# Performance work log

Hardware: AMD Instinct MI355X
Metric: run time of the kernel (lower is better)

The kernel has to match this reference:

```python
import jax, jax.numpy as jnp
import numpy as np

N_NODES, N_EDGES, D_IN, D_OUT = 50000, 800000, 64, 64
N_REL, N_TIME = 500, 1000


def setup_inputs() -> dict:
    key = jax.random.key(0)
    ks = jax.random.split(key, 14)
    xavier = lambda k, shape: jax.random.normal(k, shape, jnp.float32) * np.sqrt(2.0 / (shape[0] + shape[1])) * np.sqrt(2.0)
    return {
        "x": jax.random.normal(ks[0], (N_NODES, D_IN), jnp.float32),
        "rel_repr": jax.random.normal(ks[1], (N_REL, D_IN), jnp.float32),
        "time_emds": jax.random.normal(ks[2], (N_TIME, D_IN), jnp.float32),
        "src": jax.random.randint(ks[3], (N_EDGES,), 0, N_NODES),
        "dst": jax.random.randint(ks[4], (N_EDGES,), 0, N_NODES),
        "etype": jax.random.randint(ks[5], (N_EDGES,), 0, N_REL),
        "etime": jax.random.randint(ks[6], (N_EDGES,), 0, N_TIME),
        "trans_w": xavier(ks[7], (D_IN, D_OUT)),
        "loop_w": xavier(ks[8], (D_IN, D_OUT)),
        "w_rel": xavier(ks[9], (D_IN, D_OUT)),
        "attn_h": xavier(ks[10], (D_IN, 1)),
        "attn_t": xavier(ks[11], (D_IN, 1)),
        "attn_r": xavier(ks[12], (D_IN, 1)),
        "attn_ts": xavier(ks[13], (D_IN, 1)),
    }


def reference(x, rel_repr, time_emds, src, dst, etype, etime,
              trans_w, loop_w, w_rel, attn_h, attn_t, attn_r, attn_ts):
    n = x.shape[0]
    # per-node / per-rel / per-time scalar attention projections
    h_att = (x @ attn_h)[:, 0]          # [N]
    t_att = (x @ attn_t)[:, 0]          # [N]
    r_att = (rel_repr @ attn_r)[:, 0]   # [R]
    ts_att = (time_emds @ attn_ts)[:, 0]  # [T]
    # edge attention logits + edge_softmax grouped by destination node
    e = jax.nn.leaky_relu(h_att[src] - t_att[dst] + r_att[etype] + ts_att[etime], 0.1)  # [E]
    m = jax.ops.segment_max(e, dst, num_segments=n)
    ex = jnp.exp(e - m[dst])
    den = jax.ops.segment_sum(ex, dst, num_segments=n)
    att = (ex / den[dst])[:, None]      # [E,1]
    # message: (head + time) * (rel + time) -> trans_w -> weighted scatter-sum to dst
    time_emd = time_emds[etime]         # [E,D]
    edge_data = (x[src] + time_emd) * (rel_repr[etype] + time_emd)
    msg = (edge_data @ trans_w) * att   # [E,D_out]
    h = jax.ops.segment_sum(msg, dst, num_segments=n)
    x_out = h + x @ loop_w
    rel_out = rel_repr @ w_rel
    return (x_out, rel_out)
```

## Files before the change

kernel.cpp:

```cpp
#include <hip/hip_runtime.h>
#include <hip/hip_bf16.h>

#define N_NODES 50000
#define N_EDGES 800000
#define D 64
#define N_REL 500
#define N_TIME 1000
#define SLOTS 64
#define NODE_BLOCKS ((N_NODES + 63) / 64)
#define REL_BLOCKS  ((N_REL + 63) / 64)

#define CB 64
#define NCB ((N_NODES + CB - 1) / CB)
#define FR 64
#define NFB ((N_NODES + FR - 1) / FR)
#define SCAP 2048
#define BINCAP 8
#define BTILE 4096
#define LSLOT 48

__device__ __forceinline__ float bf2f(unsigned short u) {
    union { unsigned int i; float f; } v;
    v.i = ((unsigned int)u) << 16;
    return v.f;
}

__global__ void proj_kernel(const float* __restrict__ x,
                            const float* __restrict__ rel,
                            const float* __restrict__ tim,
                            const float* __restrict__ ah,
                            const float* __restrict__ at,
                            const float* __restrict__ ar,
                            const float* __restrict__ ats,
                            float* __restrict__ h_att, float* __restrict__ t_att,
                            float* __restrict__ r_att, float* __restrict__ ts_att,
                            unsigned short* __restrict__ x_bf,
                            int* __restrict__ cursor) {
    int gid = blockIdx.x * blockDim.x + threadIdx.x;
    if (gid < NCB) cursor[gid] = 0;
    int wave = gid >> 6;
    int lane = threadIdx.x & 63;
    const int total = N_NODES + N_REL + N_TIME;
    if (wave >= total) return;
    if (wave < N_NODES) {
        float xv = x[wave * D + lane];
        __hip_bfloat16 b = __float2bfloat16(xv);
        x_bf[wave * D + lane] = *(unsigned short*)&b;
        float s1 = xv * ah[lane];
        float s2 = xv * at[lane];
        for (int off = 32; off; off >>= 1) {
            s1 += __shfl_down(s1, off);
            s2 += __shfl_down(s2, off);
        }
        if (lane == 0) { h_att[wave] = s1; t_att[wave] = s2; }
    } else if (wave < N_NODES + N_REL) {
        int r = wave - N_NODES;
        float v = rel[r * D + lane] * ar[lane];
        for (int off = 32; off; off >>= 1) v += __shfl_down(v, off);
        if (lane == 0) r_att[r] = v;
    } else {
        int t = wave - N_NODES - N_REL;
        float v = tim[t * D + lane] * ats[lane];
        for (int off = 32; off; off >>= 1) v += __shfl_down(v, off);
        if (lane == 0) ts_att[t] = v;
    }
}

__global__ __launch_bounds__(512)
void bin_kernel(const int* __restrict__ src, const int* __restrict__ dst,
                const int* __restrict__ etype, const int* __restrict__ etime,
                const float* __restrict__ h_att, const float* __restrict__ t_att,
                const float* __restrict__ r_att, const float* __restrict__ ts_att,
                int* __restrict__ cursor, int4* __restrict__ stage) {
    __shared__ int4 bins[NCB][BINCAP];
    __shared__ int bcnt[NCB];
    int t = threadIdx.x;
    for (int k = t; k < NCB; k += 512) bcnt[k] = 0;
    __syncthreads();

    int e0 = blockIdx.x * BTILE;
    for (int j = 0; j < 8; j++) {
        int e = e0 + j * 512 + t;
        if (e < N_EDGES) {
            int s = src[e], d = dst[e], r = etype[e], tt = etime[e];
            float lg = h_att[s] - t_att[d] + r_att[r] + ts_att[tt];
            float lr = lg > 0.f ? lg : 0.1f * lg;
            float ex = __expf(lr);
            unsigned exb = __float_as_uint(ex);
            int4 rec;
            rec.x = (int)((exb & ~7u) | (unsigned)(s & 7));
            rec.y = (int)(((unsigned)(s >> 3) << 19) | ((unsigned)r << 10) | (unsigned)tt);
            rec.z = d;
            rec.w = 0;
            int k = d >> 6;
            int pos = atomicAdd(&bcnt[k], 1);
            if (pos < BINCAP) {
                bins[k][pos] = rec;
            } else {
                int g = atomicAdd(&cursor[k], 1);
                if (g < SCAP) stage[(size_t)k * SCAP + g] = rec;
            }
        }
    }
    __syncthreads();
    for (int k = t; k < NCB; k += 512) {
        int c = bcnt[k];
        if (c > BINCAP) c = BINCAP;
        if (c > 0) {
            int base = atomicAdd(&cursor[k], c);
            for (int i = 0; i < c; i++) {
                int g = base + i;
                if (g < SCAP) stage[(size_t)k * SCAP + g] = bins[k][i];
            }
        }
    }
}

__global__ __launch_bounds__(512)
void node_fused_kernel(const unsigned short* __restrict__ x_bf,
                       const float* __restrict__ rel,
                       const float* __restrict__ tim,
                       const float* __restrict__ x,
                       const float* __restrict__ trans_w,
                       const float* __restrict__ loop_w,
                       const int* __restrict__ cursor,
                       const int4* __restrict__ stage,
                       float* __restrict__ out) {
    __shared__ int2  lslot_s[FR * LSLOT];
    __shared__ int   lcnt[FR];
    __shared__ float Wt[D * D];
    __shared__ float Wl[D * D];
    __shared__ float Xt[FR * D];
    float* At = (float*)lslot_s;

    int tid = threadIdx.x;
    int base = blockIdx.x * FR;
    int pb = blockIdx.x;

    for (int i = tid; i < FR; i += 512) lcnt[i] = 0;
    {
        int2 z = make_int2(0, 0);
        for (int i = tid; i < FR * LSLOT; i += 512) lslot_s[i] = z;
    }
    for (int j = 0; j < 2; j++) {
        int idx = (tid + 512 * j) * 4;
        *(float4*)(Wt + idx) = *(const float4*)(trans_w + idx);
        *(float4*)(Wl + idx) = *(const float4*)(loop_w + idx);
    }
    for (int j = 0; j < 2; j++) {
        int lin = tid + 512 * j;
        int rr = lin >> 4;
        int k4 = (lin & 15) << 2;
        int gr = base + rr; if (gr >= N_NODES) gr = N_NODES - 1;
        *(float4*)(Xt + rr * D + k4) = *(const float4*)(x + (size_t)gr * D + k4);
    }
    __syncthreads();

    int n = cursor[pb];
    if (n > SCAP) n = SCAP;
    for (int i = tid; i < n; i += 512) {
        int4 rec = stage[(size_t)pb * SCAP + i];
        int ln = rec.z - base;
        if ((unsigned)ln < FR) {
            int pos = atomicAdd(&lcnt[ln], 1);
            if (pos < LSLOT) lslot_s[ln * LSLOT + pos] = make_int2(rec.x, rec.y);
        }
    }
    __syncthreads();

    int lane = tid & 63;
    int wv = tid >> 6;
    int qw = lane >> 4;
    int ql = lane & 15;
    float4 acc4[8];

#pragma unroll
    for (int j = 0; j < 8; j++) {
        int ln = wv + j * 8;
        int deg = lcnt[ln];
        if (deg > LSLOT) deg = LSLOT;

        float ex = 0.f;
        if (lane < deg) {
            int2 pl = lslot_s[ln * LSLOT + lane];
            ex = __uint_as_float((unsigned)pl.x & ~7u);
        }
        float den = ex;
        for (int off = 32; off; off >>= 1) den += __shfl_xor(den, off);
        float rden = 1.f / den;

        const int2* row = lslot_s + ln * LSLOT;
        float4 acc = make_float4(0.f, 0.f, 0.f, 0.f);
        for (int i = 0; i < deg; i += 8) {
            int eA = i + qw;
            int eB = i + 4 + qw;
            int2 pA = row[eA];
            int2 pB = row[eB];
            unsigned pxA = (unsigned)pA.x, pyA = (unsigned)pA.y;
            unsigned pxB = (unsigned)pB.x, pyB = (unsigned)pB.y;
            float attA = (eA < deg) ? __uint_as_float(pxA & ~7u) * rden : 0.f;
            float attB = (eB < deg) ? __uint_as_float(pxB & ~7u) * rden : 0.f;
            int sA = (int)(((pyA >> 19) << 3) | (pxA & 7u));
            int rA = (int)((pyA >> 10) & 511u);
            int tA = (int)(pyA & 1023u);
            int sB = (int)(((pyB >> 19) << 3) | (pxB & 7u));
            int rB = (int)((pyB >> 10) & 511u);
            int tB = (int)(pyB & 1023u);
            float4  teA = *(const float4*)(tim + tA * D + ql * 4);
            ushort4 xbA = *(const ushort4*)(x_bf + sA * D + ql * 4);
            float4  rlA = *(const float4*)(rel + rA * D + ql * 4);
            float4  teB = *(const float4*)(tim + tB * D + ql * 4);
            ushort4 xbB = *(const ushort4*)(x_bf + sB * D + ql * 4);
            float4  rlB = *(const float4*)(rel + rB * D + ql * 4);
            acc.x += attA * (bf2f(xbA.x) + teA.x) * (rlA.x + teA.x);
            acc.y += attA * (bf2f(xbA.y) + teA.y) * (rlA.y + teA.y);
            acc.z += attA * (bf2f(xbA.z) + teA.z) * (rlA.z + teA.z);
            acc.w += attA * (bf2f(xbA.w) + teA.w) * (rlA.w + teA.w);
            acc.x += attB * (bf2f(xbB.x) + teB.x) * (rlB.x + teB.x);
            acc.y += attB * (bf2f(xbB.y) + teB.y) * (rlB.y + teB.y);
            acc.z += attB * (bf2f(xbB.z) + teB.z) * (rlB.z + teB.z);
            acc.w += attB * (bf2f(xbB.w) + teB.w) * (rlB.w + teB.w);
        }
        for (int off = 16; off <= 32; off <<= 1) {
            acc.x += __shfl_xor(acc.x, off);
            acc.y += __shfl_xor(acc.y, off);
            acc.z += __shfl_xor(acc.z, off);
            acc.w += __shfl_xor(acc.w, off);
        }
        acc4[j] = acc;
    }
    __syncthreads();

#pragma unroll
    for (int j = 0; j < 8; j++) {
        if (qw == 0) {
            int ln = wv + j * 8;
            *(float4*)(At + ln * D + ql * 4) = acc4[j];
        }
    }
    __syncthreads();

    int c4 = ql << 2;
    int r0 = wv * 8 + qw * 2;
    float acc[2][4];
    for (int i = 0; i < 2; i++)
        for (int c = 0; c < 4; c++) acc[i][c] = 0.f;

    for (int k = 0; k < D; k += 4) {
        float wt[4][4], wl[4][4];
        for (int kk = 0; kk < 4; kk++) {
            *(float4*)&wt[kk][0] = *(const float4*)(Wt + (k + kk) * D + c4);
            *(float4*)&wl[kk][0] = *(const float4*)(Wl + (k + kk) * D + c4);
        }
        for (int i = 0; i < 2; i++) {
            float a[4], xv[4];
            *(float4*)&a[0]  = *(const float4*)(At + (r0 + i) * D + k);
            *(float4*)&xv[0] = *(const float4*)(Xt + (r0 + i) * D + k);
            for (int c = 0; c < 4; c++) {
                float s = acc[i][c];
                for (int kk = 0; kk < 4; kk++)
                    s += a[kk] * wt[kk][c] + xv[kk] * wl[kk][c];
                acc[i][c] = s;
            }
        }
    }
    for (int i = 0; i < 2; i++) {
        int gr = base + r0 + i;
        if (gr < N_NODES)
            *(float4*)(out + (size_t)gr * D + c4) = *(float4*)&acc[i][0];
    }
}

__global__ __launch_bounds__(256)
void rel_gemm_kernel(const float* __restrict__ rel,
                     const float* __restrict__ w_rel,
                     float* __restrict__ out) {
    __shared__ float Wa[D * D];
    __shared__ float At[64 * D];
    int t = threadIdx.x;
    int row0 = blockIdx.x * 64;

    for (int j = 0; j < 4; j++) {
        int idx = (t + 256 * j) * 4;
        *(float4*)(Wa + idx) = *(const float4*)(w_rel + idx);
    }
    for (int j = 0; j < 4; j++) {
        int lin = t + 256 * j;
        int rr = lin >> 4;
        int k4 = (lin & 15) << 2;
        int gr = row0 + rr; if (gr >= N_REL) gr = N_REL - 1;
        *(float4*)(At + rr * D + k4) = *(const float4*)(rel + (size_t)gr * D + k4);
    }
    __syncthreads();

    int lane = t & 63;
    int wv = t >> 6;
    int c4 = (lane & 15) << 2;
    int r0 = wv * 16 + (lane >> 4) * 4;

    float acc[4][4];
    for (int i = 0; i < 4; i++)
        for (int c = 0; c < 4; c++) acc[i][c] = 0.f;

    for (int k = 0; k < D; k += 4) {
        float wt[4][4];
        for (int kk = 0; kk < 4; kk++)
            *(float4*)&wt[kk][0] = *(const float4*)(Wa + (k + kk) * D + c4);
        for (int i = 0; i < 4; i++) {
            float a[4];
            *(float4*)&a[0] = *(const float4*)(At + (r0 + i) * D + k);
            for (int c = 0; c < 4; c++) {
                float s = acc[i][c];
                for (int kk = 0; kk < 4; kk++)
                    s += a[kk] * wt[kk][c];
                acc[i][c] = s;
            }
        }
    }
    for (int i = 0; i < 4; i++) {
        int gr = row0 + r0 + i;
        if (gr < N_REL)
            *(float4*)(out + (size_t)(N_NODES + gr) * D + c4) = *(float4*)&acc[i][0];
    }
}

__global__ void build_kernel(const int* __restrict__ src, const int* __restrict__ dst,
                             const int* __restrict__ etype, const int* __restrict__ etime,
                             const float* __restrict__ h_att, const float* __restrict__ t_att,
                             const float* __restrict__ r_att, const float* __restrict__ ts_att,
                             int* __restrict__ cnt, int2* __restrict__ payload) {
    int e = blockIdx.x * blockDim.x + threadIdx.x;
    if (e >= N_EDGES) return;
    int s = src[e], d = dst[e], r = etype[e], t = etime[e];
    float lg = h_att[s] - t_att[d] + r_att[r] + ts_att[t];
    float lr = lg > 0.f ? lg : 0.1f * lg;
    float ex = __expf(lr);
    unsigned exb = __float_as_uint(ex);
    int2 pl;
    pl.x = (int)((exb & ~7u) | (unsigned)(s & 7));
    pl.y = (int)(((unsigned)(s >> 3) << 19) | ((unsigned)r << 10) | (unsigned)t);
    int pos = atomicAdd(&cnt[d], 1);
    if (pos < SLOTS) payload[(d << 6) + pos] = pl;
}

__global__ void node_gather_kernel(const unsigned short* __restrict__ x_bf,
                                   const float* __restrict__ rel,
                                   const float* __restrict__ tim,
                                   const int* __restrict__ cnt,
                                   const int2* __restrict__ payload,
                                   float* __restrict__ agg) {
    int d = (blockIdx.x * blockDim.x + threadIdx.x) >> 6;
    int lane = threadIdx.x & 63;
    if (d >= N_NODES) return;
    int deg = cnt[d];
    if (deg > SLOTS) deg = SLOTS;
    int s_l = 0, r_l = 0, t_l = 0;
    float ex = 0.f;
    if (lane < deg) {
        int2 pl = payload[(d << 6) + lane];
        unsigned px = (unsigned)pl.x;
        unsigned py = (unsigned)pl.y;
        ex = __uint_as_float(px & ~7u);
        s_l = (int)(((py >> 19) << 3) | (px & 7u));
        r_l = (int)((py >> 10) & 511u);
        t_l = (int)(py & 1023u);
    }
    float den = ex;
    for (int off = 32; off; off >>= 1) den += __shfl_xor(den, off);
    float att_l = (lane < deg) ? ex / den : 0.f;
    int qw = lane >> 4;
    int ql = lane & 15;
    float4 acc = make_float4(0.f, 0.f, 0.f, 0.f);
    for (int i = 0; i < deg; i += 4) {
        int ei = i + qw;
        int s = __shfl(s_l, ei);
        int r = __shfl(r_l, ei);
        int t = __shfl(t_l, ei);
        float att = __shfl(att_l, ei);
        float4  te = *(const float4*)(tim + t * D + ql * 4);
        ushort4 xb = *(const ushort4*)(x_bf + s * D + ql * 4);
        float4  rl = *(const float4*)(rel + r * D + ql * 4);
        acc.x += att * (bf2f(xb.x) + te.x) * (rl.x + te.x);
        acc.y += att * (bf2f(xb.y) + te.y) * (rl.y + te.y);
        acc.z += att * (bf2f(xb.z) + te.z) * (rl.z + te.z);
        acc.w += att * (bf2f(xb.w) + te.w) * (rl.w + te.w);
    }
    for (int off = 16; off <= 32; off <<= 1) {
        acc.x += __shfl_xor(acc.x, off);
        acc.y += __shfl_xor(acc.y, off);
        acc.z += __shfl_xor(acc.z, off);
        acc.w += __shfl_xor(acc.w, off);
    }
    if (qw == 0)
        *(float4*)(agg + (d << 7) + ql * 4) = acc;
}

__global__ __launch_bounds__(256, 2)
void out_gemm_kernel(const float* __restrict__ agg,
                     const float* __restrict__ x,
                     const float* __restrict__ rel,
                     const float* __restrict__ trans_w,
                     const float* __restrict__ loop_w,
                     const float* __restrict__ w_rel,
                     float* __restrict__ out, int astride) {
    __shared__ float Wa[D * D];
    __shared__ float Wb[D * D];
    __shared__ float At[64 * D];
    __shared__ float Xt[64 * D];
    int t = threadIdx.x;
    bool nodeb = blockIdx.x < NODE_BLOCKS;
    int row0 = nodeb ? blockIdx.x * 64 : (blockIdx.x - NODE_BLOCKS) * 64;

    for (int j = 0; j < 4; j++) {
        int idx = (t + 256 * j) * 4;
        if (nodeb) {
            *(float4*)(Wa + idx) = *(const float4*)(trans_w + idx);
            *(float4*)(Wb + idx) = *(const float4*)(loop_w + idx);
        } else {
            *(float4*)(Wa + idx) = *(const float4*)(w_rel + idx);
        }
    }
    for (int j = 0; j < 4; j++) {
        int lin = t + 256 * j;
        int rr = lin >> 4;
        int k4 = (lin & 15) << 2;
        if (nodeb) {
            int gr = row0 + rr; if (gr >= N_NODES) gr = N_NODES - 1;
            *(float4*)(At + rr * D + k4) = *(const float4*)(agg + (size_t)gr * astride + k4);
            *(float4*)(Xt + rr * D + k4) = *(const float4*)(x + (size_t)gr * D + k4);
        } else {
            int gr = row0 + rr; if (gr >= N_REL) gr = N_REL - 1;
            *(float4*)(At + rr * D + k4) = *(const float4*)(rel + (size_t)gr * D + k4);
        }
    }
    __syncthreads();

    int lane = t & 63;
    int wv = t >> 6;
    int c4 = (lane & 15) << 2;
    int r0 = wv * 16 + (lane >> 4) * 4;

    float acc[4][4];
    for (int i = 0; i < 4; i++)
        for (int c = 0; c < 4; c++) acc[i][c] = 0.f;

    if (nodeb) {
        for (int k = 0; k < D; k += 4) {
            float wt[4][4], wl[4][4];
            for (int kk = 0; kk < 4; kk++) {
                *(float4*)&wt[kk][0] = *(const float4*)(Wa + (k + kk) * D + c4);
                *(float4*)&wl[kk][0] = *(const float4*)(Wb + (k + kk) * D + c4);
            }
            for (int i = 0; i < 4; i++) {
                float a[4], xv[4];
                *(float4*)&a[0]  = *(const float4*)(At + (r0 + i) * D + k);
                *(float4*)&xv[0] = *(const float4*)(Xt + (r0 + i) * D + k);
                for (int c = 0; c < 4; c++) {
                    float s = acc[i][c];
                    for (int kk = 0; kk < 4; kk++)
                        s += a[kk] * wt[kk][c] + xv[kk] * wl[kk][c];
                    acc[i][c] = s;
                }
            }
        }
        for (int i = 0; i < 4; i++) {
            int gr = row0 + r0 + i;
            if (gr < N_NODES)
                *(float4*)(out + (size_t)gr * D + c4) = *(float4*)&acc[i][0];
        }
    } else {
        for (int k = 0; k < D; k += 4) {
            float wt[4][4];
            for (int kk = 0; kk < 4; kk++)
                *(float4*)&wt[kk][0] = *(const float4*)(Wa + (k + kk) * D + c4);
            for (int i = 0; i < 4; i++) {
                float a[4];
                *(float4*)&a[0] = *(const float4*)(At + (r0 + i) * D + k);
                for (int c = 0; c < 4; c++) {
                    float s = acc[i][c];
                    for (int kk = 0; kk < 4; kk++)
                        s += a[kk] * wt[kk][c];
                    acc[i][c] = s;
                }
            }
        }
        for (int i = 0; i < 4; i++) {
            int gr = row0 + r0 + i;
            if (gr < N_REL)
                *(float4*)(out + (size_t)(N_NODES + gr) * D + c4) = *(float4*)&acc[i][0];
        }
    }
}

extern "C" void kernel_launch(void* const* d_in, const int* in_sizes, int n_in,
                              void* d_out, int out_size, void* d_ws, size_t ws_size,
                              hipStream_t stream) {
    const float* x    = (const float*)d_in[0];
    const float* rel  = (const float*)d_in[1];
    const float* tim  = (const float*)d_in[2];
    const int* src   = (const int*)d_in[3];
    const int* dst   = (const int*)d_in[4];
    const int* etype = (const int*)d_in[5];
    const int* etime = (const int*)d_in[6];
    const float* trans_w = (const float*)d_in[7];
    const float* loop_w  = (const float*)d_in[8];
    const float* w_rel   = (const float*)d_in[9];
    const float* ah  = (const float*)d_in[10];
    const float* at  = (const float*)d_in[11];
    const float* ar  = (const float*)d_in[12];
    const float* ats = (const float*)d_in[13];

    char* ws = (char*)d_ws;
    int*   cursor         = (int*)  (ws);
    int*   cnt            = (int*)  (ws);
    float* h_att          = (float*)(ws + 200064);
    float* t_att          = (float*)(ws + 400064);
    float* r_att          = (float*)(ws + 600064);
    float* ts_att         = (float*)(ws + 602064);
    float* agg            = (float*)(ws + 1000000);
    int2*  payload        = (int2*) (ws + 1000000);
    unsigned short* x_bf  = (unsigned short*)(ws + 26600000);
    int4*  stage          = (int4*) (ws + 33000000);

    float* out = (float*)d_out;

    const size_t need = 33000000ull + (size_t)NCB * SCAP * sizeof(int4);
    const bool fused = (ws_size >= need);

    if (!fused)
        hipMemsetAsync(cnt, 0, 200000, stream);

    {
        int waves = N_NODES + N_REL + N_TIME;
        proj_kernel<<<(waves + 3) / 4, 256, 0, stream>>>(
            x, rel, tim, ah, at, ar, ats,
            h_att, t_att, r_att, ts_att, x_bf, cursor);
    }
    if (fused) {
        bin_kernel<<<(N_EDGES + BTILE - 1) / BTILE, 512, 0, stream>>>(
            src, dst, etype, etime, h_att, t_att, r_att, ts_att,
            cursor, stage);
        node_fused_kernel<<<NFB, 512, 0, stream>>>(
            x_bf, rel, tim, x, trans_w, loop_w, cursor, stage, out);
        rel_gemm_kernel<<<REL_BLOCKS, 256, 0, stream>>>(rel, w_rel, out);
    } else {
        build_kernel<<<(N_EDGES + 255) / 256, 256, 0, stream>>>(
            src, dst, etype, etime, h_att, t_att, r_att, ts_att, cnt, payload);
        node_gather_kernel<<<(N_NODES + 3) / 4, 256, 0, stream>>>(
            x_bf, rel, tim, cnt, payload, agg);
        out_gemm_kernel<<<NODE_BLOCKS + REL_BLOCKS, 256, 0, stream>>>(
            agg, x, rel, trans_w, loop_w, w_rel, out, 128);
    }
}
```

Before: 189.0 us.

## Pack edge staging records into int2 and unroll gather loop by four

Edge records in the staging buffer shrink from int4 to int2 by packing the local destination index into low mantissa bits of the exp value, which halves staging traffic between the binning and node kernels. Bin tile and bin capacity are retuned, and the node kernel gets an occupancy hint. The per-node gather loop now handles 16 edges per iteration instead of 8 to expose more memory-level parallelism. Masking nine mantissa bits slightly lowers the precision of the softmax weights. LSLOT grows to 56 while degree is still clamped at 48, so the loop can read slots past 48; those reads are zero-weighted but may touch uninitialised slot data.

```diff
diff --git a/kernel.cpp b/kernel.cpp
--- a/kernel.cpp
+++ b/kernel.cpp
@@ -15,9 +15,9 @@
 #define FR 64
 #define NFB ((N_NODES + FR - 1) / FR)
 #define SCAP 2048
-#define BINCAP 8
-#define BTILE 4096
-#define LSLOT 48
+#define BINCAP 12
+#define BTILE 3072
+#define LSLOT 56
 
 __device__ __forceinline__ float bf2f(unsigned short u) {
     union { unsigned int i; float f; } v;
@@ -71,15 +71,15 @@
                 const int* __restrict__ etype, const int* __restrict__ etime,
                 const float* __restrict__ h_att, const float* __restrict__ t_att,
                 const float* __restrict__ r_att, const float* __restrict__ ts_att,
-                int* __restrict__ cursor, int4* __restrict__ stage) {
-    __shared__ int4 bins[NCB][BINCAP];
+                int* __restrict__ cursor, int2* __restrict__ stage) {
+    __shared__ int2 bins[NCB][BINCAP];
     __shared__ int bcnt[NCB];
     int t = threadIdx.x;
     for (int k = t; k < NCB; k += 512) bcnt[k] = 0;
     __syncthreads();
 
     int e0 = blockIdx.x * BTILE;
-    for (int j = 0; j < 8; j++) {
+    for (int j = 0; j < 6; j++) {
         int e = e0 + j * 512 + t;
         if (e < N_EDGES) {
             int s = src[e], d = dst[e], r = etype[e], tt = etime[e];
@@ -87,11 +87,9 @@
             float lr = lg > 0.f ? lg : 0.1f * lg;
             float ex = __expf(lr);
             unsigned exb = __float_as_uint(ex);
-            int4 rec;
-            rec.x = (int)((exb & ~7u) | (unsigned)(s & 7));
+            int2 rec;
+            rec.x = (int)((exb & ~511u) | ((unsigned)(s & 7) << 6) | (unsigned)(d & 63));
             rec.y = (int)(((unsigned)(s >> 3) << 19) | ((unsigned)r << 10) | (unsigned)tt);
-            rec.z = d;
-            rec.w = 0;
             int k = d >> 6;
             int pos = atomicAdd(&bcnt[k], 1);
             if (pos < BINCAP) {
@@ -116,7 +114,7 @@
     }
 }
 
-__global__ __launch_bounds__(512)
+__global__ __launch_bounds__(512, 4)
 void node_fused_kernel(const unsigned short* __restrict__ x_bf,
                        const float* __restrict__ rel,
                        const float* __restrict__ tim,
@@ -124,7 +122,7 @@
                        const float* __restrict__ trans_w,
                        const float* __restrict__ loop_w,
                        const int* __restrict__ cursor,
-                       const int4* __restrict__ stage,
+                       const int2* __restrict__ stage,
                        float* __restrict__ out) {
     __shared__ int2  lslot_s[FR * LSLOT];
     __shared__ int   lcnt[FR];
@@ -159,12 +157,10 @@
     int n = cursor[pb];
     if (n > SCAP) n = SCAP;
     for (int i = tid; i < n; i += 512) {
-        int4 rec = stage[(size_t)pb * SCAP + i];
-        int ln = rec.z - base;
-        if ((unsigned)ln < FR) {
-            int pos = atomicAdd(&lcnt[ln], 1);
-            if (pos < LSLOT) lslot_s[ln * LSLOT + pos] = make_int2(rec.x, rec.y);
-        }
+        int2 rec = stage[(size_t)pb * SCAP + i];
+        int ln = rec.x & 63;
+        int pos = atomicAdd(&lcnt[ln], 1);
+        if (pos < LSLOT) lslot_s[ln * LSLOT + pos] = rec;
     }
     __syncthreads();
 
@@ -174,16 +170,25 @@
     int ql = lane & 15;
     float4 acc4[8];
 
+#define DEC_S(PX, PY) ((int)((((PY) >> 19) << 3) | (((PX) >> 6) & 7u)))
+#define GATHER(E, PV, ATT, S_, R_, T_)                                       \
+        int2 PV = row[E];                                                    \
+        unsigned px##PV = (unsigned)PV.x, py##PV = (unsigned)PV.y;           \
+        float ATT = ((E) < deg) ? __uint_as_float(px##PV & ~511u) * rden : 0.f; \
+        int S_ = DEC_S(px##PV, py##PV);                                      \
+        int R_ = (int)((py##PV >> 10) & 511u);                               \
+        int T_ = (int)(py##PV & 1023u);
+
 #pragma unroll
     for (int j = 0; j < 8; j++) {
         int ln = wv + j * 8;
         int deg = lcnt[ln];
-        if (deg > LSLOT) deg = LSLOT;
+        if (deg > 48) deg = 48;
 
         float ex = 0.f;
         if (lane < deg) {
             int2 pl = lslot_s[ln * LSLOT + lane];
-            ex = __uint_as_float((unsigned)pl.x & ~7u);
+            ex = __uint_as_float((unsigned)pl.x & ~511u);
         }
         float den = ex;
         for (int off = 32; off; off >>= 1) den += __shfl_xor(den, off);
@@ -191,27 +196,23 @@
 
         const int2* row = lslot_s + ln * LSLOT;
         float4 acc = make_float4(0.f, 0.f, 0.f, 0.f);
-        for (int i = 0; i < deg; i += 8) {
-            int eA = i + qw;
-            int eB = i + 4 + qw;
-            int2 pA = row[eA];
-            int2 pB = row[eB];
-            unsigned pxA = (unsigned)pA.x, pyA = (unsigned)pA.y;
-            unsigned pxB = (unsigned)pB.x, pyB = (unsigned)pB.y;
-            float attA = (eA < deg) ? __uint_as_float(pxA & ~7u) * rden : 0.f;
-            float attB = (eB < deg) ? __uint_as_float(pxB & ~7u) * rden : 0.f;
-            int sA = (int)(((pyA >> 19) << 3) | (pxA & 7u));
-            int rA = (int)((pyA >> 10) & 511u);
-            int tA = (int)(pyA & 1023u);
-            int sB = (int)(((pyB >> 19) << 3) | (pxB & 7u));
-            int rB = (int)((pyB >> 10) & 511u);
-            int tB = (int)(pyB & 1023u);
+        for (int i = 0; i < deg; i += 16) {
+            GATHER(i + qw,      pA, attA, sA, rA, tA);
+            GATHER(i + 4 + qw,  pB, attB, sB, rB, tB);
+            GATHER(i + 8 + qw,  pC, attC, sC, rC, tC);
+            GATHER(i + 12 + qw, pD, attD, sD, rD, tD);
             float4  teA = *(const float4*)(tim + tA * D + ql * 4);
             ushort4 xbA = *(const ushort4*)(x_bf + sA * D + ql * 4);
             float4  rlA = *(const float4*)(rel + rA * D + ql * 4);
             float4  teB = *(const float4*)(tim + tB * D + ql * 4);
             ushort4 xbB = *(const ushort4*)(x_bf + sB * D + ql * 4);
             float4  rlB = *(const float4*)(rel + rB * D + ql * 4);
+            float4  teC = *(const float4*)(tim + tC * D + ql * 4);
+            ushort4 xbC = *(const ushort4*)(x_bf + sC * D + ql * 4);
+            float4  rlC = *(const float4*)(rel + rC * D + ql * 4);
+            float4  teD = *(const float4*)(tim + tD * D + ql * 4);
+            ushort4 xbD = *(const ushort4*)(x_bf + sD * D + ql * 4);
+            float4  rlD = *(const float4*)(rel + rD * D + ql * 4);
             acc.x += attA * (bf2f(xbA.x) + teA.x) * (rlA.x + teA.x);
             acc.y += attA * (bf2f(xbA.y) + teA.y) * (rlA.y + teA.y);
             acc.z += attA * (bf2f(xbA.z) + teA.z) * (rlA.z + teA.z);
@@ -220,6 +221,14 @@
             acc.y += attB * (bf2f(xbB.y) + teB.y) * (rlB.y + teB.y);
             acc.z += attB * (bf2f(xbB.z) + teB.z) * (rlB.z + teB.z);
             acc.w += attB * (bf2f(xbB.w) + teB.w) * (rlB.w + teB.w);
+            acc.x += attC * (bf2f(xbC.x) + teC.x) * (rlC.x + teC.x);
+            acc.y += attC * (bf2f(xbC.y) + teC.y) * (rlC.y + teC.y);
+            acc.z += attC * (bf2f(xbC.z) + teC.z) * (rlC.z + teC.z);
+            acc.w += attC * (bf2f(xbC.w) + teC.w) * (rlC.w + teC.w);
+            acc.x += attD * (bf2f(xbD.x) + teD.x) * (rlD.x + teD.x);
+            acc.y += attD * (bf2f(xbD.y) + teD.y) * (rlD.y + teD.y);
+            acc.z += attD * (bf2f(xbD.z) + teD.z) * (rlD.z + teD.z);
+            acc.w += attD * (bf2f(xbD.w) + teD.w) * (rlD.w + teD.w);
         }
         for (int off = 16; off <= 32; off <<= 1) {
             acc.x += __shfl_xor(acc.x, off);
@@ -229,6 +238,8 @@
         }
         acc4[j] = acc;
     }
+#undef GATHER
+#undef DEC_S
     __syncthreads();
 
 #pragma unroll
@@ -520,11 +531,11 @@
     float* agg            = (float*)(ws + 1000000);
     int2*  payload        = (int2*) (ws + 1000000);
     unsigned short* x_bf  = (unsigned short*)(ws + 26600000);
-    int4*  stage          = (int4*) (ws + 33000000);
+    int2*  stage          = (int2*) (ws + 33000000);
 
     float* out = (float*)d_out;
 
-    const size_t need = 33000000ull + (size_t)NCB * SCAP * sizeof(int4);
+    const size_t need = 33000000ull + (size_t)NCB * SCAP * sizeof(int2);
     const bool fused = (ws_size >= need);
 
     if (!fused)
```

New measurement: 192.9 us. 1.02x slower.
